# Kernel tuning notes

Measured on AMD Instinct MI355X. Metric: run time of the kernel, lower is better.

Reference implementation:

```python
import jax, jax.numpy as jnp
import numpy as np
import math

B, S, H = 2, 2048, 2048
NH, NKV, HD = 16, 8, 128          # heads, kv heads, head_dim
GROUPS = NH // NKV                 # 2
FF = 5632
EPS = 1e-6
SCALE = 0.02


def setup_inputs() -> dict:
    key = jax.random.key(0)
    ks = jax.random.split(key, 12)
    def w(k, shape):
        return jax.random.normal(k, shape, dtype=jnp.float32) * SCALE
    # additive causal mask: 0 on/below diagonal, -inf above
    causal = jnp.where(jnp.tril(jnp.ones((S, S), dtype=bool)), 0.0, -jnp.inf)
    attention_mask = causal[None, None].astype(jnp.float32)  # [1,1,S,S]
    return {
        "hidden_states": jax.random.normal(ks[0], (B, S, H), dtype=jnp.float32),
        "attention_mask": attention_mask,
        "q_w": w(ks[1], (NH * HD, H)),      # nn.Linear convention [out, in]
        "k_w": w(ks[2], (NKV * HD, H)),
        "v_w": w(ks[3], (NKV * HD, H)),
        "o_w": w(ks[4], (H, NH * HD)),
        "gate_w": w(ks[5], (FF, H)),
        "up_w": w(ks[6], (FF, H)),
        "down_w": w(ks[7], (H, FF)),
        "ln1_w": jnp.ones((H,), dtype=jnp.float32),
        "ln2_w": jnp.ones((H,), dtype=jnp.float32),
    }


def rmsnorm(x, w):
    var = jnp.mean(jnp.square(x), axis=-1, keepdims=True)
    return x * jax.lax.rsqrt(var + EPS) * w


def attention(x, mask, q_w, k_w, v_w, o_w):
    b, s, _ = x.shape
    q = (x @ q_w.T).reshape(b, s, NH, HD).transpose(0, 2, 1, 3)    # [b,nh,s,hd]
    k = (x @ k_w.T).reshape(b, s, NKV, HD).transpose(0, 2, 1, 3)   # [b,nkv,s,hd]
    v = (x @ v_w.T).reshape(b, s, NKV, HD).transpose(0, 2, 1, 3)
    # GQA: repeat_interleave kv heads to match query heads
    k = jnp.repeat(k, GROUPS, axis=1)
    v = jnp.repeat(v, GROUPS, axis=1)
    scores = jnp.einsum("bhqd,bhkd->bhqk", q, k) / math.sqrt(HD) + mask
    probs = jax.nn.softmax(scores.astype(jnp.float32), axis=-1).astype(q.dtype)
    out = jnp.einsum("bhqk,bhkd->bhqd", probs, v)
    out = out.transpose(0, 2, 1, 3).reshape(b, s, NH * HD)
    return out @ o_w.T


def mlp(x, gate_w, up_w, down_w):
    return (jax.nn.silu(x @ gate_w.T) * (x @ up_w.T)) @ down_w.T


def reference(hidden_states, attention_mask, q_w, k_w, v_w, o_w,
              gate_w, up_w, down_w, ln1_w, ln2_w):
    # pre-norm transformer layer with residuals
    h = hidden_states + attention(rmsnorm(hidden_states, ln1_w), attention_mask,
                                  q_w, k_w, v_w, o_w)
    out = h + mlp(rmsnorm(h, ln2_w), gate_w, up_w, down_w)
    return out
```

## Files before the change

kernel.cpp:

```cpp
#include <hip/hip_runtime.h>
#include <stdint.h>

typedef __bf16 bf16_t;
typedef __bf16 bf16x8 __attribute__((ext_vector_type(8)));
typedef __bf16 bf16x4 __attribute__((ext_vector_type(4)));
typedef float  f32x4  __attribute__((ext_vector_type(4)));

#define MFMA16(a, b, c) __builtin_amdgcn_mfma_f32_16x16x32_bf16((a), (b), (c), 0, 0, 0)

__device__ __forceinline__ void load_lds16(const bf16_t* g, bf16_t* l)
{
    __builtin_amdgcn_global_load_lds(
        (const __attribute__((address_space(1))) uint32_t*)(uintptr_t)g,
        (__attribute__((address_space(3))) uint32_t*)(uint32_t)(uintptr_t)l,
        16, 0, 0);
}

__device__ __forceinline__ void lds_stage2(const bf16_t* __restrict__ Gsrc,
                                           bf16_t* Ldst, int u0,
                                           int tid, int K, int k0)
{
#pragma unroll
    for (int l = 0; l < 2; ++l) {
        int u = u0 + l * 512 + tid;
        int row = u >> 3;
        int col = (((u & 7) ^ (row & 7)) << 3);
        load_lds16(Gsrc + (size_t)row * K + k0 + col, Ldst + u * 8);
    }
}

__global__ __launch_bounds__(256)
void wconv_all(const float* __restrict__ qw, const float* __restrict__ kw,
               const float* __restrict__ vw, const float* __restrict__ ow,
               const float* __restrict__ gw, const float* __restrict__ uw,
               const float* __restrict__ dw, bf16_t* __restrict__ ws)
{
    const int blk = blockIdx.x;
    const float* src; bf16_t* dst; int off;
    if      (blk <  2048) { src = qw; dst = ws;            off = blk;         }
    else if (blk <  3072) { src = kw; dst = ws +  4194304; off = blk -  2048; }
    else if (blk <  4096) { src = vw; dst = ws +  6291456; off = blk -  3072; }
    else if (blk <  6144) { src = ow; dst = ws +  8388608; off = blk -  4096; }
    else if (blk < 11776) { src = gw; dst = ws + 12582912; off = blk -  6144; }
    else if (blk < 17408) { src = uw; dst = ws + 24117248; off = blk - 11776; }
    else                  { src = dw; dst = ws + 35651584; off = blk - 17408; }

    int i = (off * 256 + threadIdx.x) * 8;
    f32x4 a = *(const f32x4*)(src + i);
    f32x4 b = *(const f32x4*)(src + i + 4);
    bf16x8 y;
#pragma unroll
    for (int e = 0; e < 4; ++e) { y[e] = (bf16_t)a[e]; y[e + 4] = (bf16_t)b[e]; }
    *(bf16x8*)(dst + i) = y;
}

__global__ __launch_bounds__(256)
void rmsnorm_f32(const float* __restrict__ X, const float* __restrict__ Wt,
                 bf16_t* __restrict__ Y)
{
    __shared__ float red[4];
    const int tid = threadIdx.x;
    const size_t row = blockIdx.x;
    const float* x = X + row * 2048;

    f32x4 x0 = *(const f32x4*)(x + tid * 8);
    f32x4 x1 = *(const f32x4*)(x + tid * 8 + 4);
    float ss = 0.f;
#pragma unroll
    for (int e = 0; e < 4; ++e) ss += x0[e] * x0[e] + x1[e] * x1[e];
#pragma unroll
    for (int off = 32; off; off >>= 1) ss += __shfl_xor(ss, off, 64);
    if ((tid & 63) == 0) red[tid >> 6] = ss;
    __syncthreads();
    float tot = red[0] + red[1] + red[2] + red[3];
    float scale = rsqrtf(tot * (1.f / 2048.f) + 1e-6f);

    f32x4 w0 = *(const f32x4*)(Wt + tid * 8);
    f32x4 w1 = *(const f32x4*)(Wt + tid * 8 + 4);
    bf16x8 yv;
#pragma unroll
    for (int e = 0; e < 4; ++e) {
        yv[e]     = (bf16_t)(x0[e] * scale * w0[e]);
        yv[e + 4] = (bf16_t)(x1[e] * scale * w1[e]);
    }
    *(bf16x8*)(Y + row * 2048 + tid * 8) = yv;
}

__global__ __launch_bounds__(256)
void rmsnorm_bf16(const bf16_t* __restrict__ X, const float* __restrict__ Wt,
                  bf16_t* __restrict__ Y)
{
    __shared__ float red[4];
    const int tid = threadIdx.x;
    const size_t row = blockIdx.x;

    bf16x8 xv = *(const bf16x8*)(X + row * 2048 + tid * 8);
    float xf[8];
    float ss = 0.f;
#pragma unroll
    for (int e = 0; e < 8; ++e) { xf[e] = (float)xv[e]; ss += xf[e] * xf[e]; }
#pragma unroll
    for (int off = 32; off; off >>= 1) ss += __shfl_xor(ss, off, 64);
    if ((tid & 63) == 0) red[tid >> 6] = ss;
    __syncthreads();
    float tot = red[0] + red[1] + red[2] + red[3];
    float scale = rsqrtf(tot * (1.f / 2048.f) + 1e-6f);

    f32x4 w0 = *(const f32x4*)(Wt + tid * 8);
    f32x4 w1 = *(const f32x4*)(Wt + tid * 8 + 4);
    bf16x8 yv;
#pragma unroll
    for (int e = 0; e < 4; ++e) {
        yv[e]     = (bf16_t)(xf[e] * scale * w0[e]);
        yv[e + 4] = (bf16_t)(xf[e + 4] * scale * w1[e]);
    }
    *(bf16x8*)(Y + row * 2048 + tid * 8) = yv;
}

__global__ __launch_bounds__(512, 1)
void gemm_qkv(const bf16_t* __restrict__ A, const bf16_t* __restrict__ W,
              bf16_t* __restrict__ Qb, bf16_t* __restrict__ Kb,
              bf16_t* __restrict__ Vb, int K)
{
    __shared__ bf16_t As[2][256 * 64];
    __shared__ bf16_t Ws[2][256 * 64];

    const int tid  = threadIdx.x;
    const int lane = tid & 63, wave = tid >> 6;
    const int quad = lane >> 4, l16 = lane & 15;
    const int wr = wave >> 2, wc = wave & 3;

    const int lid = (int)blockIdx.x;
    const int swz = (lid & 7) * 32 + (lid >> 3);
    const int bym = swz & 15, bxn = swz >> 4;
    const int m0 = bym * 256, n0 = bxn * 256;

    const bf16_t* Ab = A + (size_t)m0 * K;
    const bf16_t* Wb = W + (size_t)n0 * K;

    const int xsw  = (l16 & 7) << 3;
    const int aoff = (wr * 128 + l16) * 64;
    const int boff = (wc * 64 + l16) * 64;

    f32x4 acc[8][4] = {};

    lds_stage2(Ab, As[0], 0,    tid, K, 0);
    lds_stage2(Ab, As[0], 1024, tid, K, 0);
    lds_stage2(Wb, Ws[0], 0,    tid, K, 0);
    lds_stage2(Wb, Ws[0], 1024, tid, K, 0);

    const int NT = K >> 6;
    for (int t = 0; t < NT; ++t) {
        const int b  = t & 1;
        const int kn = (t + 1) << 6;
        const bool pf = (t + 1 < NT);
        bf16_t* An = As[1 - b];
        bf16_t* Wn = Ws[1 - b];

        if (pf) {
            lds_stage2(Ab, An, 0, tid, K, kn);
            asm volatile("s_waitcnt vmcnt(2)" ::: "memory");
        } else {
            asm volatile("s_waitcnt vmcnt(0)" ::: "memory");
        }
        __builtin_amdgcn_s_barrier();

        const bf16_t* Asb = As[b];
        const bf16_t* Wsb = Ws[b];
        bf16x8 af[4], bb[4];

        {
            const int kxo = (quad * 8) ^ xsw;
#pragma unroll
            for (int i = 0; i < 4; ++i)
                af[i] = *(const bf16x8*)(Asb + aoff + i * 1024 + kxo);
#pragma unroll
            for (int j = 0; j < 4; ++j)
                bb[j] = *(const bf16x8*)(Wsb + boff + j * 1024 + kxo);
        }
        if (pf) lds_stage2(Ab, An, 1024, tid, K, kn);
        __builtin_amdgcn_s_barrier();
        __builtin_amdgcn_s_setprio(1);
#pragma unroll
        for (int i = 0; i < 4; ++i)
#pragma unroll
            for (int j = 0; j < 4; ++j)
                acc[i][j] = MFMA16(af[i], bb[j], acc[i][j]);
        __builtin_amdgcn_s_setprio(0);
        __builtin_amdgcn_s_barrier();

        {
            const int kxo = (quad * 8) ^ xsw;
#pragma unroll
            for (int i = 0; i < 4; ++i)
                af[i] = *(const bf16x8*)(Asb + aoff + (i + 4) * 1024 + kxo);
        }
        if (pf) lds_stage2(Wb, Wn, 0, tid, K, kn);
        __builtin_amdgcn_s_barrier();
        __builtin_amdgcn_s_setprio(1);
#pragma unroll
        for (int i = 0; i < 4; ++i)
#pragma unroll
            for (int j = 0; j < 4; ++j)
                acc[i + 4][j] = MFMA16(af[i], bb[j], acc[i + 4][j]);
        __builtin_amdgcn_s_setprio(0);
        __builtin_amdgcn_s_barrier();

        {
            const int kxo = (32 + quad * 8) ^ xsw;
#pragma unroll
            for (int i = 0; i < 4; ++i)
                af[i] = *(const bf16x8*)(Asb + aoff + i * 1024 + kxo);
#pragma unroll
            for (int j = 0; j < 4; ++j)
                bb[j] = *(const bf16x8*)(Wsb + boff + j * 1024 + kxo);
        }
        if (pf) lds_stage2(Wb, Wn, 1024, tid, K, kn);
        __builtin_amdgcn_s_barrier();
        __builtin_amdgcn_s_setprio(1);
#pragma unroll
        for (int i = 0; i < 4; ++i)
#pragma unroll
            for (int j = 0; j < 4; ++j)
                acc[i][j] = MFMA16(af[i], bb[j], acc[i][j]);
        __builtin_amdgcn_s_setprio(0);
        __builtin_amdgcn_s_barrier();

        {
            const int kxo = (32 + quad * 8) ^ xsw;
#pragma unroll
            for (int i = 0; i < 4; ++i)
                af[i] = *(const bf16x8*)(Asb + aoff + (i + 4) * 1024 + kxo);
        }
        __builtin_amdgcn_s_barrier();
        __builtin_amdgcn_s_setprio(1);
#pragma unroll
        for (int i = 0; i < 4; ++i)
#pragma unroll
            for (int j = 0; j < 4; ++j)
                acc[i + 4][j] = MFMA16(af[i], bb[j], acc[i + 4][j]);
        __builtin_amdgcn_s_setprio(0);
        __builtin_amdgcn_s_barrier();
    }

#pragma unroll
    for (int i = 0; i < 8; ++i)
#pragma unroll
        for (int j = 0; j < 4; ++j)
#pragma unroll
            for (int r = 0; r < 4; ++r) {
                size_t row = (size_t)(m0 + wr * 128 + i * 16 + quad * 4 + r);
                int    col = n0 + wc * 64 + j * 16 + l16;
                bf16_t v = (bf16_t)acc[i][j][r];
                if (col < 2048)      Qb[row * 2048 + col] = v;
                else if (col < 3072) Kb[row * 1024 + (col - 2048)] = v;
                else                 Vb[row * 1024 + (col - 3072)] = v;
            }
}

__global__ __launch_bounds__(512, 2)
void gemm8(const bf16_t* __restrict__ A, const bf16_t* __restrict__ W,
           const float* __restrict__ Rf, const bf16_t* __restrict__ Rb,
           bf16_t* __restrict__ Cb, float* __restrict__ Cf,
           int M, int N, int K, int nbx, int mode)
{
    __shared__ bf16_t As[2][256 * 64];
    __shared__ bf16_t Ws[2][128 * 64];

    const int tid  = threadIdx.x;
    const int lane = tid & 63, wave = tid >> 6;
    const int quad = lane >> 4, l16 = lane & 15;
    const int wr = wave >> 1, wc = wave & 1;

    const int lid = (int)blockIdx.x;
    const int nwg = (M >> 8) * nbx;
    const int q   = nwg >> 3;
    const int swz = (lid & 7) * q + (lid >> 3);
    const int bxn = swz >> 4;
    const int bym = swz & 15;
    const int m0 = bym * 256, n0 = bxn * 128;

    const bf16_t* Ab = A + (size_t)m0 * K;
    const bf16_t* Wb = W + (size_t)n0 * K;

    const int xsw  = (l16 & 7) << 3;
    const int aoff = (wr * 64 + l16) * 64;
    const int boff = (wc * 64 + l16) * 64;

    f32x4 acc[4][4] = {};

    lds_stage2(Ab, As[0], 0,    tid, K, 0);
    lds_stage2(Ab, As[0], 1024, tid, K, 0);
    lds_stage2(Wb, Ws[0], 0,    tid, K, 0);

    const int NT = K >> 6;
    for (int t = 0; t < NT; ++t) {
        const int b  = t & 1;
        const int kn = (t + 1) << 6;
        const bool pf = (t + 1 < NT);
        bf16_t* An = As[1 - b];
        bf16_t* Wn = Ws[1 - b];

        if (pf) {
            lds_stage2(Ab, An, 0, tid, K, kn);
            asm volatile("s_waitcnt vmcnt(2)" ::: "memory");
        } else {
            asm volatile("s_waitcnt vmcnt(0)" ::: "memory");
        }
        __builtin_amdgcn_s_barrier();

        const bf16_t* Asb = As[b];
        const bf16_t* Wsb = Ws[b];

#pragma unroll
        for (int ks = 0; ks < 2; ++ks) {
            const int kxo = (ks * 32 + quad * 8) ^ xsw;
            bf16x8 af[4], bf_[4];
#pragma unroll
            for (int i = 0; i < 4; ++i)
                af[i] = *(const bf16x8*)(Asb + aoff + i * 1024 + kxo);
#pragma unroll
            for (int j = 0; j < 4; ++j)
                bf_[j] = *(const bf16x8*)(Wsb + boff + j * 1024 + kxo);
            if (pf) {
                if (ks == 0) lds_stage2(Ab, An, 1024, tid, K, kn);
                else         lds_stage2(Wb, Wn, 0,    tid, K, kn);
            }
            __builtin_amdgcn_s_barrier();
            __builtin_amdgcn_s_setprio(1);
#pragma unroll
            for (int i = 0; i < 4; ++i)
#pragma unroll
                for (int j = 0; j < 4; ++j)
                    acc[i][j] = MFMA16(af[i], bf_[j], acc[i][j]);
            __builtin_amdgcn_s_setprio(0);
            __builtin_amdgcn_s_barrier();
        }
    }

#pragma unroll
    for (int i = 0; i < 4; ++i)
#pragma unroll
        for (int j = 0; j < 4; ++j)
#pragma unroll
            for (int r = 0; r < 4; ++r) {
                size_t row = (size_t)(m0 + wr * 64 + i * 16 + quad * 4 + r);
                size_t col = (size_t)(n0 + wc * 64 + j * 16 + l16);
                float v = acc[i][j][r];
                if (mode == 1) v += Rf[row * (size_t)N + col];
                if (mode == 2)
                    Cf[row * (size_t)N + col] = v + (float)Rb[row * (size_t)N + col];
                else
                    Cb[row * (size_t)N + col] = (bf16_t)v;
            }
}

__global__ __launch_bounds__(512, 2)
void gateup8(const bf16_t* __restrict__ A, const bf16_t* __restrict__ G,
             const bf16_t* __restrict__ U, bf16_t* __restrict__ C,
             int M, int N, int K)
{
    __shared__ bf16_t As[2][256 * 64];
    __shared__ bf16_t Gs[2][128 * 64];
    __shared__ bf16_t Us[2][128 * 64];

    const int tid  = threadIdx.x;
    const int lane = tid & 63;
    const int wave = tid >> 6;
    const int quad = lane >> 4, l16 = lane & 15;
    const int wr = wave >> 2, wc = wave & 3;

    const int lid = (int)blockIdx.x;
    const int nwg = (M >> 8) * (N >> 7);
    const int cpx = nwg >> 3;
    const int swz = (lid & 7) * cpx + (lid >> 3);
    const int bxn = swz >> 4;
    const int bym = swz & 15;
    const int m0 = bym * 256, n0 = bxn * 128;

    const bf16_t* Ab = A + (size_t)m0 * K;
    const bf16_t* Gb = G + (size_t)n0 * K;
    const bf16_t* Ub = U + (size_t)n0 * K;

    const int xsw  = (l16 & 7) << 3;
    const int aoff = (wr * 128 + l16) * 64;
    const int boff = (wc * 32 + l16) * 64;

    f32x4 accg[8][2] = {};
    f32x4 accu[8][2] = {};

    lds_stage2(Ab, As[0], 0,    tid, K, 0);
    lds_stage2(Ab, As[0], 1024, tid, K, 0);
    lds_stage2(Gb, Gs[0], 0,    tid, K, 0);
    lds_stage2(Ub, Us[0], 0,    tid, K, 0);

    const int NT = K >> 6;
    for (int t = 0; t < NT; ++t) {
        const int b  = t & 1;
        const int kn = (t + 1) << 6;
        const bool pf = (t + 1 < NT);
        bf16_t* An = As[1 - b];
        bf16_t* Gn = Gs[1 - b];
        bf16_t* Un = Us[1 - b];

        if (pf) {
            lds_stage2(Ab, An, 0, tid, K, kn);
            asm volatile("s_waitcnt vmcnt(2)" ::: "memory");
        } else {
            asm volatile("s_waitcnt vmcnt(0)" ::: "memory");
        }
        __builtin_amdgcn_s_barrier();

        const bf16_t* Asb = As[b];
        const bf16_t* Gsb = Gs[b];
        const bf16_t* Usb = Us[b];

        bf16x8 af[4], bg[2], bu[2];

        {
            const int kxo = (quad * 8) ^ xsw;
#pragma unroll
            for (int i = 0; i < 4; ++i)
                af[i] = *(const bf16x8*)(Asb + aoff + i * 1024 + kxo);
#pragma unroll
            for (int j = 0; j < 2; ++j) {
                bg[j] = *(const bf16x8*)(Gsb + boff + j * 1024 + kxo);
                bu[j] = *(const bf16x8*)(Usb + boff + j * 1024 + kxo);
            }
        }
        if (pf) lds_stage2(Ab, An, 1024, tid, K, kn);
        __builtin_amdgcn_s_barrier();
        __builtin_amdgcn_s_setprio(1);
#pragma unroll
        for (int i = 0; i < 4; ++i)
#pragma unroll
            for (int j = 0; j < 2; ++j) {
                accg[i][j] = MFMA16(af[i], bg[j], accg[i][j]);
                accu[i][j] = MFMA16(af[i], bu[j], accu[i][j]);
            }
        __builtin_amdgcn_s_setprio(0);
        __builtin_amdgcn_s_barrier();

        {
            const int kxo = (quad * 8) ^ xsw;
#pragma unroll
            for (int i = 0; i < 4; ++i)
                af[i] = *(const bf16x8*)(Asb + aoff + (i + 4) * 1024 + kxo);
        }
        if (pf) lds_stage2(Gb, Gn, 0, tid, K, kn);
        __builtin_amdgcn_s_barrier();
        __builtin_amdgcn_s_setprio(1);
#pragma unroll
        for (int i = 0; i < 4; ++i)
#pragma unroll
            for (int j = 0; j < 2; ++j) {
                accg[i + 4][j] = MFMA16(af[i], bg[j], accg[i + 4][j]);
                accu[i + 4][j] = MFMA16(af[i], bu[j], accu[i + 4][j]);
            }
        __builtin_amdgcn_s_setprio(0);
        __builtin_amdgcn_s_barrier();

        {
            const int kxo = (32 + quad * 8) ^ xsw;
#pragma unroll
            for (int i = 0; i < 4; ++i)
                af[i] = *(const bf16x8*)(Asb + aoff + i * 1024 + kxo);
#pragma unroll
            for (int j = 0; j < 2; ++j) {
                bg[j] = *(const bf16x8*)(Gsb + boff + j * 1024 + kxo);
                bu[j] = *(const bf16x8*)(Usb + boff + j * 1024 + kxo);
            }
        }
        if (pf) lds_stage2(Ub, Un, 0, tid, K, kn);
        __builtin_amdgcn_s_barrier();
        __builtin_amdgcn_s_setprio(1);
#pragma unroll
        for (int i = 0; i < 4; ++i)
#pragma unroll
            for (int j = 0; j < 2; ++j) {
                accg[i][j] = MFMA16(af[i], bg[j], accg[i][j]);
                accu[i][j] = MFMA16(af[i], bu[j], accu[i][j]);
            }
        __builtin_amdgcn_s_setprio(0);
        __builtin_amdgcn_s_barrier();

        {
            const int kxo = (32 + quad * 8) ^ xsw;
#pragma unroll
            for (int i = 0; i < 4; ++i)
                af[i] = *(const bf16x8*)(Asb + aoff + (i + 4) * 1024 + kxo);
        }
        __builtin_amdgcn_s_barrier();
        __builtin_amdgcn_s_setprio(1);
#pragma unroll
        for (int i = 0; i < 4; ++i)
#pragma unroll
            for (int j = 0; j < 2; ++j) {
                accg[i + 4][j] = MFMA16(af[i], bg[j], accg[i + 4][j]);
                accu[i + 4][j] = MFMA16(af[i], bu[j], accu[i + 4][j]);
            }
        __builtin_amdgcn_s_setprio(0);
        __builtin_amdgcn_s_barrier();
    }

#pragma unroll
    for (int i = 0; i < 8; ++i)
#pragma unroll
        for (int j = 0; j < 2; ++j)
#pragma unroll
            for (int r = 0; r < 4; ++r) {
                size_t row = (size_t)(m0 + wr * 128 + i * 16 + quad * 4 + r);
                size_t col = (size_t)(n0 + wc * 32 + j * 16 + l16);
                float g = accg[i][j][r];
                float u = accu[i][j][r];
                float sig = 1.f / (1.f + __expf(fminf(-g, 80.f)));
                C[row * (size_t)N + col] = (bf16_t)(g * sig * u);
            }
}

__global__ __launch_bounds__(256, 2)
void gemm_bt(const bf16_t* __restrict__ A, const float* __restrict__ W,
             const float* __restrict__ Rf, const bf16_t* __restrict__ Rb,
             bf16_t* __restrict__ Cb, float* __restrict__ Cf,
             int M, int N, int K, int mode)
{
    __shared__ bf16_t As[128 * 64];
    __shared__ bf16_t Ws[128 * 64];

    const int tid  = threadIdx.x;
    const int lane = tid & 63, wave = tid >> 6;
    const int quad = lane >> 4, l16 = lane & 15;
    const int m0 = blockIdx.y * 128, n0 = blockIdx.x * 128;
    const int wm = (wave >> 1) * 64, wn = (wave & 1) * 64;

    f32x4 acc[4][4] = {};

    for (int k0 = 0; k0 < K; k0 += 64) {
        bf16x8 ra[4];
        bf16x4 rw[8];
#pragma unroll
        for (int i = 0; i < 4; ++i) {
            int u = i * 256 + tid;
            int r = u >> 3, c = (u & 7) << 3;
            ra[i] = *(const bf16x8*)(A + (size_t)(m0 + r) * K + k0 + c);
        }
#pragma unroll
        for (int i = 0; i < 8; ++i) {
            int u = i * 256 + tid;
            int r = u >> 4, c = (u & 15) << 2;
            f32x4 w4 = *(const f32x4*)(W + (size_t)(n0 + r) * K + k0 + c);
#pragma unroll
            for (int e = 0; e < 4; ++e) rw[i][e] = (bf16_t)w4[e];
        }
        __syncthreads();
#pragma unroll
        for (int i = 0; i < 4; ++i)
            *(bf16x8*)(As + (i * 256 + tid) * 8) = ra[i];
#pragma unroll
        for (int i = 0; i < 8; ++i)
            *(bf16x4*)(Ws + (i * 256 + tid) * 4) = rw[i];
        __syncthreads();

#pragma unroll
        for (int ks = 0; ks < 64; ks += 32) {
            bf16x8 af[4], bfr[4];
#pragma unroll
            for (int i = 0; i < 4; ++i)
                af[i] = *(const bf16x8*)(As + (wm + i * 16 + l16) * 64 + ks + quad * 8);
#pragma unroll
            for (int j = 0; j < 4; ++j)
                bfr[j] = *(const bf16x8*)(Ws + (wn + j * 16 + l16) * 64 + ks + quad * 8);
#pragma unroll
            for (int i = 0; i < 4; ++i)
#pragma unroll
                for (int j = 0; j < 4; ++j)
                    acc[i][j] = MFMA16(af[i], bfr[j], acc[i][j]);
        }
    }

#pragma unroll
    for (int i = 0; i < 4; ++i)
#pragma unroll
        for (int j = 0; j < 4; ++j)
#pragma unroll
            for (int r = 0; r < 4; ++r) {
                size_t row = (size_t)(m0 + wm + i * 16 + quad * 4 + r);
                size_t col = (size_t)(n0 + wn + j * 16 + l16);
                float v = acc[i][j][r];
                if (mode == 1) v += Rf[row * (size_t)N + col];
                if (mode == 2)
                    Cf[row * (size_t)N + col] = v + (float)Rb[row * (size_t)N + col];
                else
                    Cb[row * (size_t)N + col] = (bf16_t)v;
            }
}

__global__ __launch_bounds__(256, 2)
void gemm_gateup(const bf16_t* __restrict__ A, const float* __restrict__ G,
                 const float* __restrict__ U, bf16_t* __restrict__ C,
                 int M, int N, int K)
{
    __shared__ bf16_t As[128 * 64];
    __shared__ bf16_t Gs[128 * 64];
    __shared__ bf16_t Us[128 * 64];

    const int tid  = threadIdx.x;
    const int lane = tid & 63, wave = tid >> 6;
    const int quad = lane >> 4, l16 = lane & 15;
    const int m0 = blockIdx.y * 128, n0 = blockIdx.x * 128;
    const int wm = (wave >> 1) * 64, wn = (wave & 1) * 64;

    f32x4 accg[4][4] = {};
    f32x4 accu[4][4] = {};

    for (int k0 = 0; k0 < K; k0 += 64) {
        bf16x8 ra[4];
        bf16x4 rg[8], ru[8];
#pragma unroll
        for (int i = 0; i < 4; ++i) {
            int u = i * 256 + tid;
            int r = u >> 3, c = (u & 7) << 3;
            ra[i] = *(const bf16x8*)(A + (size_t)(m0 + r) * K + k0 + c);
        }
#pragma unroll
        for (int i = 0; i < 8; ++i) {
            int u = i * 256 + tid;
            int r = u >> 4, c = (u & 15) << 2;
            f32x4 g4 = *(const f32x4*)(G + (size_t)(n0 + r) * K + k0 + c);
            f32x4 u4 = *(const f32x4*)(U + (size_t)(n0 + r) * K + k0 + c);
#pragma unroll
            for (int e = 0; e < 4; ++e) { rg[i][e] = (bf16_t)g4[e]; ru[i][e] = (bf16_t)u4[e]; }
        }
        __syncthreads();
#pragma unroll
        for (int i = 0; i < 4; ++i)
            *(bf16x8*)(As + (i * 256 + tid) * 8) = ra[i];
#pragma unroll
        for (int i = 0; i < 8; ++i) {
            *(bf16x4*)(Gs + (i * 256 + tid) * 4) = rg[i];
            *(bf16x4*)(Us + (i * 256 + tid) * 4) = ru[i];
        }
        __syncthreads();

#pragma unroll
        for (int ks = 0; ks < 64; ks += 32) {
            bf16x8 af[4], bg[4], bu[4];
#pragma unroll
            for (int i = 0; i < 4; ++i)
                af[i] = *(const bf16x8*)(As + (wm + i * 16 + l16) * 64 + ks + quad * 8);
#pragma unroll
            for (int j = 0; j < 4; ++j) {
                bg[j] = *(const bf16x8*)(Gs + (wn + j * 16 + l16) * 64 + ks + quad * 8);
                bu[j] = *(const bf16x8*)(Us + (wn + j * 16 + l16) * 64 + ks + quad * 8);
            }
#pragma unroll
            for (int i = 0; i < 4; ++i)
#pragma unroll
                for (int j = 0; j < 4; ++j) {
                    accg[i][j] = MFMA16(af[i], bg[j], accg[i][j]);
                    accu[i][j] = MFMA16(af[i], bu[j], accu[i][j]);
                }
        }
    }

#pragma unroll
    for (int i = 0; i < 4; ++i)
#pragma unroll
        for (int j = 0; j < 4; ++j)
#pragma unroll
            for (int r = 0; r < 4; ++r) {
                size_t row = (size_t)(m0 + wm + i * 16 + quad * 4 + r);
                size_t col = (size_t)(n0 + wn + j * 16 + l16);
                float g = accg[i][j][r];
                float u = accu[i][j][r];
                float sig = 1.f / (1.f + __expf(fminf(-g, 80.f)));
                C[row * (size_t)N + col] = (bf16_t)(g * sig * u);
            }
}

__global__ __launch_bounds__(256, 2)
void attn_fwd(const bf16_t* __restrict__ Q, const bf16_t* __restrict__ Kg,
              const bf16_t* __restrict__ Vg, bf16_t* __restrict__ O, int kvs)
{
    __shared__ bf16_t Ks[2][64 * 128];
    __shared__ bf16_t Vt[2][128 * 64];
    __shared__ bf16_t Pl[4][16 * 72];

    const int tid  = threadIdx.x;
    const int lane = tid & 63, wave = tid >> 6;
    const int quad = lane >> 4, l16 = lane & 15;
    const int bh = blockIdx.y, b = bh >> 4, h = bh & 15;

    const bf16_t* Qh = Q  + (size_t)b * 2048 * 2048 + (size_t)h * 128;
    const bf16_t* Kh = Kg + (size_t)b * 2048 * kvs + (size_t)(h >> 1) * 128;
    const bf16_t* Vh = Vg + (size_t)b * 2048 * kvs + (size_t)(h >> 1) * 128;

    const float scale = 0.08838834764831845f;

    const int krow = tid >> 4;
    const int kcol = (tid & 15) << 3;
    const int vd   = tid & 127;
    const int vkb  = tid >> 7;

#pragma unroll 1
    for (int pass = 0; pass < 2; ++pass) {
        const int qt = pass ? (31 - (int)blockIdx.x) : (int)blockIdx.x;
        const int q0 = qt * 64;

        bf16x8 aq[4];
#pragma unroll
        for (int ks = 0; ks < 4; ++ks)
            aq[ks] = *(const bf16x8*)(Qh + (size_t)(q0 + wave * 16 + l16) * 2048 + ks * 32 + quad * 8);

        float m_r[4] = { -30000.f, -30000.f, -30000.f, -30000.f };
        float l_r[4] = { 0.f, 0.f, 0.f, 0.f };
        f32x4 acc_o[8] = {};

        const int ntiles = qt + 1;

        bf16x8 rk[4], rv[4];
#pragma unroll
        for (int i = 0; i < 4; ++i)
            rk[i] = *(const bf16x8*)(Kh + (size_t)(i * 16 + krow) * kvs + kcol);
#pragma unroll
        for (int it = 0; it < 4; ++it)
#pragma unroll
            for (int j = 0; j < 8; ++j)
                rv[it][j] = Vh[(size_t)((vkb + 2 * it) * 8 + j) * kvs + vd];
#pragma unroll
        for (int i = 0; i < 4; ++i) {
            int row = i * 16 + krow;
            *(bf16x8*)(&Ks[0][row * 128 + (kcol ^ ((row & 7) << 3))]) = rk[i];
        }
#pragma unroll
        for (int it = 0; it < 4; ++it) {
            int kb = vkb + 2 * it;
            *(bf16x8*)(&Vt[0][vd * 64 + ((kb ^ (vd & 7)) << 3)]) = rv[it];
        }
        __syncthreads();

        for (int t = 0; t < ntiles; ++t) {
            const int bb = t & 1;
            const bool pf = (t + 1 < ntiles);
            const bool diag = (t == qt);
            const int kv0 = t * 64;
            const int kvn = kv0 + 64;

            if (pf) {
#pragma unroll
                for (int i = 0; i < 4; ++i)
                    rk[i] = *(const bf16x8*)(Kh + (size_t)(kvn + i * 16 + krow) * kvs + kcol);
#pragma unroll
                for (int it = 0; it < 4; ++it)
#pragma unroll
                    for (int j = 0; j < 8; ++j)
                        rv[it][j] = Vh[(size_t)(kvn + (vkb + 2 * it) * 8 + j) * kvs + vd];
            }

            f32x4 accs[4] = {};
            __builtin_amdgcn_s_setprio(1);
#pragma unroll
            for (int ks = 0; ks < 4; ++ks)
#pragma unroll
                for (int j = 0; j < 4; ++j) {
                    const int row = j * 16 + l16;
                    bf16x8 bk = *(const bf16x8*)(&Ks[bb][row * 128 + ((ks * 32 + quad * 8) ^ ((row & 7) << 3))]);
                    accs[j] = MFMA16(aq[ks], bk, accs[j]);
                }
            __builtin_amdgcn_s_setprio(0);

#pragma unroll
            for (int r = 0; r < 4; ++r) {
                const int qrow = q0 + wave * 16 + quad * 4 + r;
                float s[4];
#pragma unroll
                for (int j = 0; j < 4; ++j) s[j] = accs[j][r] * scale;
                if (diag) {
#pragma unroll
                    for (int j = 0; j < 4; ++j)
                        if (kv0 + j * 16 + l16 > qrow) s[j] = -30000.f;
                }
                float mx = fmaxf(fmaxf(s[0], s[1]), fmaxf(s[2], s[3]));
                mx = fmaxf(mx, __shfl_xor(mx, 1, 64));
                mx = fmaxf(mx, __shfl_xor(mx, 2, 64));
                mx = fmaxf(mx, __shfl_xor(mx, 4, 64));
                mx = fmaxf(mx, __shfl_xor(mx, 8, 64));
                float mnew  = fmaxf(m_r[r], mx);
                float alpha = __expf(fmaxf(m_r[r] - mnew, -80.f));
                float rs = 0.f;
#pragma unroll
                for (int j = 0; j < 4; ++j) {
                    float p = __expf(fmaxf(s[j] - mnew, -80.f));
                    rs += p;
                    Pl[wave][(quad * 4 + r) * 72 + j * 16 + l16] = (bf16_t)p;
                }
                rs += __shfl_xor(rs, 1, 64);
                rs += __shfl_xor(rs, 2, 64);
                rs += __shfl_xor(rs, 4, 64);
                rs += __shfl_xor(rs, 8, 64);
                l_r[r] = l_r[r] * alpha + rs;
                m_r[r] = mnew;
#pragma unroll
                for (int nt = 0; nt < 8; ++nt) acc_o[nt][r] *= alpha;
            }

            __builtin_amdgcn_s_setprio(1);
#pragma unroll
            for (int ks2 = 0; ks2 < 2; ++ks2) {
                bf16x8 ap = *(const bf16x8*)(&Pl[wave][l16 * 72 + ks2 * 32 + quad * 8]);
                const int kb_r = ks2 * 4 + quad;
#pragma unroll
                for (int nt = 0; nt < 8; ++nt) {
                    const int d = nt * 16 + l16;
                    bf16x8 bv = *(const bf16x8*)(&Vt[bb][d * 64 + ((kb_r ^ (d & 7)) << 3)]);
                    acc_o[nt] = MFMA16(ap, bv, acc_o[nt]);
                }
            }
            __builtin_amdgcn_s_setprio(0);

            if (pf) {
#pragma unroll
                for (int i = 0; i < 4; ++i) {
                    int row = i * 16 + krow;
                    *(bf16x8*)(&Ks[1 - bb][row * 128 + (kcol ^ ((row & 7) << 3))]) = rk[i];
                }
#pragma unroll
                for (int it = 0; it < 4; ++it) {
                    int kb = vkb + 2 * it;
                    *(bf16x8*)(&Vt[1 - bb][vd * 64 + ((kb ^ (vd & 7)) << 3)]) = rv[it];
                }
            }
            __syncthreads();
        }

#pragma unroll
        for (int r = 0; r < 4; ++r) {
            float inv = 1.f / fmaxf(l_r[r], 1e-30f);
            size_t orow = (size_t)b * 2048 + q0 + wave * 16 + quad * 4 + r;
#pragma unroll
            for (int nt = 0; nt < 8; ++nt)
                O[orow * 2048 + h * 128 + nt * 16 + l16] = (bf16_t)(acc_o[nt][r] * inv);
        }
    }
}

extern "C" void kernel_launch(void* const* d_in, const int* in_sizes, int n_in,
                              void* d_out, int out_size, void* d_ws, size_t ws_size,
                              hipStream_t stream)
{
    const float* x   = (const float*)d_in[0];
    const float* qw  = (const float*)d_in[2];
    const float* kw  = (const float*)d_in[3];
    const float* vw  = (const float*)d_in[4];
    const float* ow  = (const float*)d_in[5];
    const float* gw  = (const float*)d_in[6];
    const float* uw  = (const float*)d_in[7];
    const float* dw  = (const float*)d_in[8];
    const float* ln1 = (const float*)d_in[9];
    const float* ln2 = (const float*)d_in[10];
    float*  out = (float*)d_out;
    bf16_t* ws  = (bf16_t*)d_ws;

    dim3 blk(256);
    const size_t NEED = 87031808ull * 2;

    if (ws_size >= NEED) {
        bf16_t* wq = ws;
        bf16_t* wo = ws + 8388608;
        bf16_t* wg = ws + 12582912;
        bf16_t* wu = ws + 24117248;
        bf16_t* wd = ws + 35651584;
        bf16_t* h1 = ws + 47185920;
        bf16_t* qb = ws + 55574528;
        bf16_t* kb = ws + 63963136;
        bf16_t* vb = ws + 68157440;
        bf16_t* ab = (bf16_t*)d_out;
        bf16_t* hb = qb;
        bf16_t* gb = kb;

        wconv_all<<<23040, blk, 0, stream>>>(qw, kw, vw, ow, gw, uw, dw, ws);
        rmsnorm_f32<<<4096, blk, 0, stream>>>(x, ln1, h1);
        gemm_qkv<<<256, dim3(512), 0, stream>>>(h1, wq, qb, kb, vb, 2048);
        attn_fwd<<<dim3(16, 32), blk, 0, stream>>>(qb, kb, vb, ab, 1024);
        gemm8<<<256, dim3(512), 0, stream>>>(ab, wo, x, nullptr, hb, nullptr, 4096, 2048, 2048, 16, 1);
        rmsnorm_bf16<<<4096, blk, 0, stream>>>(hb, ln2, h1);
        gateup8<<<704, dim3(512), 0, stream>>>(h1, wg, wu, gb, 4096, 5632, 2048);
        gemm8<<<256, dim3(512), 0, stream>>>(gb, wd, nullptr, hb, nullptr, out, 4096, 2048, 5632, 16, 2);
    } else {
        const size_t ME = 1ull << 20;
        bf16_t* h1 = ws;
        bf16_t* qb = ws + 8  * ME;
        bf16_t* kb = ws + 16 * ME;
        bf16_t* vb = ws + 20 * ME;
        bf16_t* ab = (bf16_t*)d_out;
        bf16_t* hb = ws + 8  * ME;
        bf16_t* gb = ws + 16 * ME;

        rmsnorm_f32<<<4096, blk, 0, stream>>>(x, ln1, h1);
        gemm_bt<<<dim3(16, 32), blk, 0, stream>>>(h1, qw, nullptr, nullptr, qb, nullptr, 4096, 2048, 2048, 0);
        gemm_bt<<<dim3( 8, 32), blk, 0, stream>>>(h1, kw, nullptr, nullptr, kb, nullptr, 4096, 1024, 2048, 0);
        gemm_bt<<<dim3( 8, 32), blk, 0, stream>>>(h1, vw, nullptr, nullptr, vb, nullptr, 4096, 1024, 2048, 0);
        attn_fwd<<<dim3(16, 32), blk, 0, stream>>>(qb, kb, vb, ab, 1024);
        gemm_bt<<<dim3(16, 32), blk, 0, stream>>>(ab, ow, x, nullptr, hb, nullptr, 4096, 2048, 2048, 1);
        rmsnorm_bf16<<<4096, blk, 0, stream>>>(hb, ln2, h1);
        gemm_gateup<<<dim3(44, 32), blk, 0, stream>>>(h1, gw, uw, gb, 4096, 5632, 2048);
        gemm_bt<<<dim3(16, 32), blk, 0, stream>>>(gb, dw, nullptr, hb, nullptr, out, 4096, 2048, 5632, 2);
    }
}
```

Baseline: 787.4 us.

## Interleave gate/up weights and fuse into single 256-wide gate-up GEMM

The weight conversion kernel now interleaves gate and up rows in 16-row groups into one combined matrix. A new gateup_il kernel treats that matrix as a single B operand with 256-wide N tiles and applies SiLU-multiply on adjacent 16-column pairs in the epilogue. It replaces gateup8, which staged separate gate and up tiles. The goal is a simpler, uniform MFMA loop with fewer distinct LDS streams, at the cost of launch bounds that drop from 2 blocks per CU to 1, which lowers occupancy.

```diff
diff --git a/kernel.cpp b/kernel.cpp
--- a/kernel.cpp
+++ b/kernel.cpp
@@ -36,22 +36,24 @@
                const float* __restrict__ dw, bf16_t* __restrict__ ws)
 {
     const int blk = blockIdx.x;
-    const float* src; bf16_t* dst; int off;
-    if      (blk <  2048) { src = qw; dst = ws;            off = blk;         }
-    else if (blk <  3072) { src = kw; dst = ws +  4194304; off = blk -  2048; }
-    else if (blk <  4096) { src = vw; dst = ws +  6291456; off = blk -  3072; }
-    else if (blk <  6144) { src = ow; dst = ws +  8388608; off = blk -  4096; }
-    else if (blk < 11776) { src = gw; dst = ws + 12582912; off = blk -  6144; }
-    else if (blk < 17408) { src = uw; dst = ws + 24117248; off = blk - 11776; }
-    else                  { src = dw; dst = ws + 35651584; off = blk - 17408; }
-
-    int i = (off * 256 + threadIdx.x) * 8;
-    f32x4 a = *(const f32x4*)(src + i);
-    f32x4 b = *(const f32x4*)(src + i + 4);
+    const float* src; bf16_t* dst; size_t srow, drow;
+    if      (blk <  2048) { src = qw; dst = ws;            srow = blk;         drow = srow; }
+    else if (blk <  3072) { src = kw; dst = ws +  4194304; srow = blk -  2048; drow = srow; }
+    else if (blk <  4096) { src = vw; dst = ws +  6291456; srow = blk -  3072; drow = srow; }
+    else if (blk <  6144) { src = ow; dst = ws +  8388608; srow = blk -  4096; drow = srow; }
+    else if (blk < 11776) { src = gw; dst = ws + 12582912; srow = blk -  6144;
+                            drow = 32 * (srow >> 4) + (srow & 15); }
+    else if (blk < 17408) { src = uw; dst = ws + 12582912; srow = blk - 11776;
+                            drow = 32 * (srow >> 4) + 16 + (srow & 15); }
+    else                  { src = dw; dst = ws + 35651584; srow = blk - 17408; drow = srow; }
+
+    int c = threadIdx.x * 8;
+    f32x4 a = *(const f32x4*)(src + srow * 2048 + c);
+    f32x4 b = *(const f32x4*)(src + srow * 2048 + c + 4);
     bf16x8 y;
 #pragma unroll
     for (int e = 0; e < 4; ++e) { y[e] = (bf16_t)a[e]; y[e + 4] = (bf16_t)b[e]; }
-    *(bf16x8*)(dst + i) = y;
+    *(bf16x8*)(dst + drow * 2048 + c) = y;
 }
 
 __global__ __launch_bounds__(256)
@@ -255,6 +257,147 @@
                 if (col < 2048)      Qb[row * 2048 + col] = v;
                 else if (col < 3072) Kb[row * 1024 + (col - 2048)] = v;
                 else                 Vb[row * 1024 + (col - 3072)] = v;
+            }
+}
+
+__global__ __launch_bounds__(512, 1)
+void gateup_il(const bf16_t* __restrict__ A, const bf16_t* __restrict__ W,
+               bf16_t* __restrict__ C, int K)
+{
+    __shared__ bf16_t As[2][256 * 64];
+    __shared__ bf16_t Ws[2][256 * 64];
+
+    const int tid  = threadIdx.x;
+    const int lane = tid & 63, wave = tid >> 6;
+    const int quad = lane >> 4, l16 = lane & 15;
+    const int wr = wave >> 2, wc = wave & 3;
+
+    const int lid = (int)blockIdx.x;
+    const int swz = (lid & 7) * 88 + (lid >> 3);
+    const int bxn = swz >> 4;
+    const int bym = swz & 15;
+    const int m0 = bym * 256, n0 = bxn * 256;
+
+    const bf16_t* Ab = A + (size_t)m0 * K;
+    const bf16_t* Wb = W + (size_t)n0 * K;
+
+    const int xsw  = (l16 & 7) << 3;
+    const int aoff = (wr * 128 + l16) * 64;
+    const int boff = (wc * 64 + l16) * 64;
+
+    f32x4 acc[8][4] = {};
+
+    lds_stage2(Ab, As[0], 0,    tid, K, 0);
+    lds_stage2(Ab, As[0], 1024, tid, K, 0);
+    lds_stage2(Wb, Ws[0], 0,    tid, K, 0);
+    lds_stage2(Wb, Ws[0], 1024, tid, K, 0);
+
+    const int NT = K >> 6;
+    for (int t = 0; t < NT; ++t) {
+        const int b  = t & 1;
+        const int kn = (t + 1) << 6;
+        const bool pf = (t + 1 < NT);
+        bf16_t* An = As[1 - b];
+        bf16_t* Wn = Ws[1 - b];
+
+        if (pf) {
+            lds_stage2(Ab, An, 0, tid, K, kn);
+            asm volatile("s_waitcnt vmcnt(2)" ::: "memory");
+        } else {
+            asm volatile("s_waitcnt vmcnt(0)" ::: "memory");
+        }
+        __builtin_amdgcn_s_barrier();
+
+        const bf16_t* Asb = As[b];
+        const bf16_t* Wsb = Ws[b];
+        bf16x8 af[4], bb[4];
+
+        {
+            const int kxo = (quad * 8) ^ xsw;
+#pragma unroll
+            for (int i = 0; i < 4; ++i)
+                af[i] = *(const bf16x8*)(Asb + aoff + i * 1024 + kxo);
+#pragma unroll
+            for (int j = 0; j < 4; ++j)
+                bb[j] = *(const bf16x8*)(Wsb + boff + j * 1024 + kxo);
+        }
+        if (pf) lds_stage2(Ab, An, 1024, tid, K, kn);
+        __builtin_amdgcn_s_barrier();
+        __builtin_amdgcn_s_setprio(1);
+#pragma unroll
+        for (int i = 0; i < 4; ++i)
+#pragma unroll
+            for (int j = 0; j < 4; ++j)
+                acc[i][j] = MFMA16(af[i], bb[j], acc[i][j]);
+        __builtin_amdgcn_s_setprio(0);
+        __builtin_amdgcn_s_barrier();
+
+        {
+            const int kxo = (quad * 8) ^ xsw;
+#pragma unroll
+            for (int i = 0; i < 4; ++i)
+                af[i] = *(const bf16x8*)(Asb + aoff + (i + 4) * 1024 + kxo);
+        }
+        if (pf) lds_stage2(Wb, Wn, 0, tid, K, kn);
+        __builtin_amdgcn_s_barrier();
+        __builtin_amdgcn_s_setprio(1);
+#pragma unroll
+        for (int i = 0; i < 4; ++i)
+#pragma unroll
+            for (int j = 0; j < 4; ++j)
+                acc[i + 4][j] = MFMA16(af[i], bb[j], acc[i + 4][j]);
+        __builtin_amdgcn_s_setprio(0);
+        __builtin_amdgcn_s_barrier();
+
+        {
+            const int kxo = (32 + quad * 8) ^ xsw;
+#pragma unroll
+            for (int i = 0; i < 4; ++i)
+                af[i] = *(const bf16x8*)(Asb + aoff + i * 1024 + kxo);
+#pragma unroll
+            for (int j = 0; j < 4; ++j)
+                bb[j] = *(const bf16x8*)(Wsb + boff + j * 1024 + kxo);
+        }
+        if (pf) lds_stage2(Wb, Wn, 1024, tid, K, kn);
+        __builtin_amdgcn_s_barrier();
+        __builtin_amdgcn_s_setprio(1);
+#pragma unroll
+        for (int i = 0; i < 4; ++i)
+#pragma unroll
+            for (int j = 0; j < 4; ++j)
+                acc[i][j] = MFMA16(af[i], bb[j], acc[i][j]);
+        __builtin_amdgcn_s_setprio(0);
+        __builtin_amdgcn_s_barrier();
+
+        {
+            const int kxo = (32 + quad * 8) ^ xsw;
+#pragma unroll
+            for (int i = 0; i < 4; ++i)
+                af[i] = *(const bf16x8*)(Asb + aoff + (i + 4) * 1024 + kxo);
+        }
+        __builtin_amdgcn_s_barrier();
+        __builtin_amdgcn_s_setprio(1);
+#pragma unroll
+        for (int i = 0; i < 4; ++i)
+#pragma unroll
+            for (int j = 0; j < 4; ++j)
+                acc[i + 4][j] = MFMA16(af[i], bb[j], acc[i + 4][j]);
+        __builtin_amdgcn_s_setprio(0);
+        __builtin_amdgcn_s_barrier();
+    }
+
+#pragma unroll
+    for (int i = 0; i < 8; ++i)
+#pragma unroll
+        for (int jp = 0; jp < 2; ++jp)
+#pragma unroll
+            for (int r = 0; r < 4; ++r) {
+                size_t row = (size_t)(m0 + wr * 128 + i * 16 + quad * 4 + r);
+                size_t col = (size_t)((n0 >> 1) + wc * 32 + jp * 16 + l16);
+                float g = acc[i][2 * jp][r];
+                float u = acc[i][2 * jp + 1][r];
+                float sig = 1.f / (1.f + __expf(fminf(-g, 80.f)));
+                C[row * 5632 + col] = (bf16_t)(g * sig * u);
             }
 }
 
@@ -352,169 +495,6 @@
                     Cf[row * (size_t)N + col] = v + (float)Rb[row * (size_t)N + col];
                 else
                     Cb[row * (size_t)N + col] = (bf16_t)v;
-            }
-}
-
-__global__ __launch_bounds__(512, 2)
-void gateup8(const bf16_t* __restrict__ A, const bf16_t* __restrict__ G,
-             const bf16_t* __restrict__ U, bf16_t* __restrict__ C,
-             int M, int N, int K)
-{
-    __shared__ bf16_t As[2][256 * 64];
-    __shared__ bf16_t Gs[2][128 * 64];
-    __shared__ bf16_t Us[2][128 * 64];
-
-    const int tid  = threadIdx.x;
-    const int lane = tid & 63;
-    const int wave = tid >> 6;
-    const int quad = lane >> 4, l16 = lane & 15;
-    const int wr = wave >> 2, wc = wave & 3;
-
-    const int lid = (int)blockIdx.x;
-    const int nwg = (M >> 8) * (N >> 7);
-    const int cpx = nwg >> 3;
-    const int swz = (lid & 7) * cpx + (lid >> 3);
-    const int bxn = swz >> 4;
-    const int bym = swz & 15;
-    const int m0 = bym * 256, n0 = bxn * 128;
-
-    const bf16_t* Ab = A + (size_t)m0 * K;
-    const bf16_t* Gb = G + (size_t)n0 * K;
-    const bf16_t* Ub = U + (size_t)n0 * K;
-
-    const int xsw  = (l16 & 7) << 3;
-    const int aoff = (wr * 128 + l16) * 64;
-    const int boff = (wc * 32 + l16) * 64;
-
-    f32x4 accg[8][2] = {};
-    f32x4 accu[8][2] = {};
-
-    lds_stage2(Ab, As[0], 0,    tid, K, 0);
-    lds_stage2(Ab, As[0], 1024, tid, K, 0);
-    lds_stage2(Gb, Gs[0], 0,    tid, K, 0);
-    lds_stage2(Ub, Us[0], 0,    tid, K, 0);
-
-    const int NT = K >> 6;
-    for (int t = 0; t < NT; ++t) {
-        const int b  = t & 1;
-        const int kn = (t + 1) << 6;
-        const bool pf = (t + 1 < NT);
-        bf16_t* An = As[1 - b];
-        bf16_t* Gn = Gs[1 - b];
-        bf16_t* Un = Us[1 - b];
-
-        if (pf) {
-            lds_stage2(Ab, An, 0, tid, K, kn);
-            asm volatile("s_waitcnt vmcnt(2)" ::: "memory");
-        } else {
-            asm volatile("s_waitcnt vmcnt(0)" ::: "memory");
-        }
-        __builtin_amdgcn_s_barrier();
-
-        const bf16_t* Asb = As[b];
-        const bf16_t* Gsb = Gs[b];
-        const bf16_t* Usb = Us[b];
-
-        bf16x8 af[4], bg[2], bu[2];
-
-        {
-            const int kxo = (quad * 8) ^ xsw;
-#pragma unroll
-            for (int i = 0; i < 4; ++i)
-                af[i] = *(const bf16x8*)(Asb + aoff + i * 1024 + kxo);
-#pragma unroll
-            for (int j = 0; j < 2; ++j) {
-                bg[j] = *(const bf16x8*)(Gsb + boff + j * 1024 + kxo);
-                bu[j] = *(const bf16x8*)(Usb + boff + j * 1024 + kxo);
-            }
-        }
-        if (pf) lds_stage2(Ab, An, 1024, tid, K, kn);
-        __builtin_amdgcn_s_barrier();
-        __builtin_amdgcn_s_setprio(1);
-#pragma unroll
-        for (int i = 0; i < 4; ++i)
-#pragma unroll
-            for (int j = 0; j < 2; ++j) {
-                accg[i][j] = MFMA16(af[i], bg[j], accg[i][j]);
-                accu[i][j] = MFMA16(af[i], bu[j], accu[i][j]);
-            }
-        __builtin_amdgcn_s_setprio(0);
-        __builtin_amdgcn_s_barrier();
-
-        {
-            const int kxo = (quad * 8) ^ xsw;
-#pragma unroll
-            for (int i = 0; i < 4; ++i)
-                af[i] = *(const bf16x8*)(Asb + aoff + (i + 4) * 1024 + kxo);
-        }
-        if (pf) lds_stage2(Gb, Gn, 0, tid, K, kn);
-        __builtin_amdgcn_s_barrier();
-        __builtin_amdgcn_s_setprio(1);
-#pragma unroll
-        for (int i = 0; i < 4; ++i)
-#pragma unroll
-            for (int j = 0; j < 2; ++j) {
-                accg[i + 4][j] = MFMA16(af[i], bg[j], accg[i + 4][j]);
-                accu[i + 4][j] = MFMA16(af[i], bu[j], accu[i + 4][j]);
-            }
-        __builtin_amdgcn_s_setprio(0);
-        __builtin_amdgcn_s_barrier();
-
-        {
-            const int kxo = (32 + quad * 8) ^ xsw;
-#pragma unroll
-            for (int i = 0; i < 4; ++i)
-                af[i] = *(const bf16x8*)(Asb + aoff + i * 1024 + kxo);
-#pragma unroll
-            for (int j = 0; j < 2; ++j) {
-                bg[j] = *(const bf16x8*)(Gsb + boff + j * 1024 + kxo);
-                bu[j] = *(const bf16x8*)(Usb + boff + j * 1024 + kxo);
-            }
-        }
-        if (pf) lds_stage2(Ub, Un, 0, tid, K, kn);
-        __builtin_amdgcn_s_barrier();
-        __builtin_amdgcn_s_setprio(1);
-#pragma unroll
-        for (int i = 0; i < 4; ++i)
-#pragma unroll
-            for (int j = 0; j < 2; ++j) {
-                accg[i][j] = MFMA16(af[i], bg[j], accg[i][j]);
-                accu[i][j] = MFMA16(af[i], bu[j], accu[i][j]);
-            }
-        __builtin_amdgcn_s_setprio(0);
-        __builtin_amdgcn_s_barrier();
-
-        {
-            const int kxo = (32 + quad * 8) ^ xsw;
-#pragma unroll
-            for (int i = 0; i < 4; ++i)
-                af[i] = *(const bf16x8*)(Asb + aoff + (i + 4) * 1024 + kxo);
-        }
-        __builtin_amdgcn_s_barrier();
-        __builtin_amdgcn_s_setprio(1);
-#pragma unroll
-        for (int i = 0; i < 4; ++i)
-#pragma unroll
-            for (int j = 0; j < 2; ++j) {
-                accg[i + 4][j] = MFMA16(af[i], bg[j], accg[i + 4][j]);
-                accu[i + 4][j] = MFMA16(af[i], bu[j], accu[i + 4][j]);
-            }
-        __builtin_amdgcn_s_setprio(0);
-        __builtin_amdgcn_s_barrier();
-    }
-
-#pragma unroll
-    for (int i = 0; i < 8; ++i)
-#pragma unroll
-        for (int j = 0; j < 2; ++j)
-#pragma unroll
-            for (int r = 0; r < 4; ++r) {
-                size_t row = (size_t)(m0 + wr * 128 + i * 16 + quad * 4 + r);
-                size_t col = (size_t)(n0 + wc * 32 + j * 16 + l16);
-                float g = accg[i][j][r];
-                float u = accu[i][j][r];
-                float sig = 1.f / (1.f + __expf(fminf(-g, 80.f)));
-                C[row * (size_t)N + col] = (bf16_t)(g * sig * u);
             }
 }
 
@@ -865,18 +845,17 @@
     const size_t NEED = 87031808ull * 2;
 
     if (ws_size >= NEED) {
-        bf16_t* wq = ws;
-        bf16_t* wo = ws + 8388608;
-        bf16_t* wg = ws + 12582912;
-        bf16_t* wu = ws + 24117248;
-        bf16_t* wd = ws + 35651584;
-        bf16_t* h1 = ws + 47185920;
-        bf16_t* qb = ws + 55574528;
-        bf16_t* kb = ws + 63963136;
-        bf16_t* vb = ws + 68157440;
-        bf16_t* ab = (bf16_t*)d_out;
-        bf16_t* hb = qb;
-        bf16_t* gb = kb;
+        bf16_t* wq  = ws;
+        bf16_t* wo  = ws + 8388608;
+        bf16_t* wgu = ws + 12582912;
+        bf16_t* wd  = ws + 35651584;
+        bf16_t* h1  = ws + 47185920;
+        bf16_t* qb  = ws + 55574528;
+        bf16_t* kb  = ws + 63963136;
+        bf16_t* vb  = ws + 68157440;
+        bf16_t* ab  = (bf16_t*)d_out;
+        bf16_t* hb  = qb;
+        bf16_t* gb  = kb;
 
         wconv_all<<<23040, blk, 0, stream>>>(qw, kw, vw, ow, gw, uw, dw, ws);
         rmsnorm_f32<<<4096, blk, 0, stream>>>(x, ln1, h1);
@@ -884,7 +863,7 @@
         attn_fwd<<<dim3(16, 32), blk, 0, stream>>>(qb, kb, vb, ab, 1024);
         gemm8<<<256, dim3(512), 0, stream>>>(ab, wo, x, nullptr, hb, nullptr, 4096, 2048, 2048, 16, 1);
         rmsnorm_bf16<<<4096, blk, 0, stream>>>(hb, ln2, h1);
-        gateup8<<<704, dim3(512), 0, stream>>>(h1, wg, wu, gb, 4096, 5632, 2048);
+        gateup_il<<<704, dim3(512), 0, stream>>>(h1, wgu, gb, 2048);
         gemm8<<<256, dim3(512), 0, stream>>>(gb, wd, nullptr, hb, nullptr, out, 4096, 2048, 5632, 16, 2);
     } else {
         const size_t ME = 1ull << 20;
```

New measurement: 777.9 us. No clear change (-1.2%).
